# Kernel optimization log

Hardware: AMD Instinct MI355X
Metric: run time of the kernel (lower is better)

Reference implementation:

```python
import jax, jax.numpy as jnp
import numpy as np

NUM_HEADS = 8
KEY_SIZE = 64
VALUE_SIZE = 64
NUM_GROUPS = 3 * NUM_HEADS  # 24
C = NUM_HEADS * (2 * KEY_SIZE + VALUE_SIZE)  # 1536
EPS = 1e-5


def setup_inputs() -> dict:
    key = jax.random.key(0)
    k1, k2, k3 = jax.random.split(key, 3)
    x = jax.random.normal(k1, (8, C, 32, 32), dtype=jnp.float32)
    # GroupNorm affine params (torch default ones/zeros, perturbed for non-trivial grads)
    gn_weight = 1.0 + 0.1 * jax.random.normal(k2, (C,), dtype=jnp.float32)
    gn_bias = 0.1 * jax.random.normal(k3, (C,), dtype=jnp.float32)
    return {"x": x, "gn_weight": gn_weight, "gn_bias": gn_bias}


def _group_norm(x, weight, bias):
    B, Cc, H, W = x.shape
    xg = x.reshape(B, NUM_GROUPS, -1)  # [B, G, (C/G)*H*W]
    mean = jnp.mean(xg, axis=-1, keepdims=True)
    var = jnp.var(xg, axis=-1, keepdims=True)
    xn = ((xg - mean) * jax.lax.rsqrt(var + EPS)).reshape(B, Cc, H, W)
    return xn * weight[:, None, None] + bias[:, None, None]


def reference(x, gn_weight, gn_bias):
    NH, KS, VS = NUM_HEADS, KEY_SIZE, VALUE_SIZE
    B, Cc, H, W = x.shape
    xn = _group_norm(x, gn_weight, gn_bias)
    xr = xn.reshape(B, NH, 2 * KS + VS, H * W)  # [B, NH, 2KS+VS, NK]
    k = xr[:, :, :KS]            # [B, NH, KS, NK]
    q = xr[:, :, KS:2 * KS]      # [B, NH, KS, NK]
    v = xr[:, :, 2 * KS:]        # [B, NH, VS, NK]
    # saliency = q^T @ k / sqrt(KS) -> [B, NH, NKq, NKk]
    sal = jnp.einsum('bhcq,bhck->bhqk', q, k) / jnp.sqrt(jnp.float32(KS))
    mask = jax.nn.softmax(sal, axis=-1)
    # out = v @ mask^T -> [B, NH, VS, NKq]
    out = jnp.einsum('bhvk,bhqk->bhvq', v, mask)
    return out.reshape(B, NH * VS, H, W)
```

## Files before the change

### kernel.cpp

```cpp
#include <hip/hip_runtime.h>
#include <hip/hip_bf16.h>


typedef __attribute__((ext_vector_type(8))) short bf16x8;
typedef __attribute__((ext_vector_type(4))) float f32x4;
typedef __attribute__((ext_vector_type(16))) float f32x16;
typedef unsigned short u16;
typedef unsigned int u32;

#define SM_SCALE 0.18033688f
#define SM_OFF   8.0f

__device__ __forceinline__ u32 pack2(float a, float b) {
    union { float f; u32 u; } ua, ub; ua.f = a; ub.f = b;
    return __builtin_amdgcn_perm(ub.u + 0x8000u, ua.u + 0x8000u, 0x07060302u);
}
union BB { uint4 u; bf16x8 v; };

__device__ __forceinline__ float fexp2(float x) {
#if __has_builtin(__builtin_amdgcn_exp2f)
    return __builtin_amdgcn_exp2f(x);
#else
    float r; asm("v_exp_f32 %0, %1" : "=v"(r) : "v"(x)); return r;
#endif
}

__device__ __forceinline__ f32x16 zero16() {
    f32x16 z;
#pragma unroll
    for (int i = 0; i < 16; ++i) z[i] = 0.f;
    return z;
}

__device__ __forceinline__ void swap32(u32 a, u32 b, int hi, u32& ret0, u32& ret1) {
#if __has_builtin(__builtin_amdgcn_permlane32_swap)
    (void)hi;
    auto sw = __builtin_amdgcn_permlane32_swap(a, b, false, false);
    ret0 = sw[0]; ret1 = sw[1];
#else
    u32 pa = __shfl_xor(a, 32), pb = __shfl_xor(b, 32);
    ret0 = hi ? pb : a;
    ret1 = hi ? b : pa;
#endif
}

__global__ __launch_bounds__(256) void gn_partial(const float* __restrict__ x,
                                                  float* __restrict__ partials) {
    int blk = blockIdx.x;
    const float4* p = (const float4*)(x + (size_t)blk * 8192);
    int t = threadIdx.x;
    float s1a = 0.f, s2a = 0.f, s1b = 0.f, s2b = 0.f;
#pragma unroll
    for (int i = 0; i < 8; i += 2) {
        float4 va = p[t + i * 256];
        float4 vb = p[t + (i + 1) * 256];
        s1a += va.x + va.y + va.z + va.w;
        s2a += va.x*va.x + va.y*va.y + va.z*va.z + va.w*va.w;
        s1b += vb.x + vb.y + vb.z + vb.w;
        s2b += vb.x*vb.x + vb.y*vb.y + vb.z*vb.z + vb.w*vb.w;
    }
    float s1 = s1a + s1b, s2 = s2a + s2b;
    for (int off = 32; off > 0; off >>= 1) {
        s1 += __shfl_down(s1, off);
        s2 += __shfl_down(s2, off);
    }
    __shared__ float a1[4], a2[4];
    int wave = t >> 6, lane = t & 63;
    if (lane == 0) { a1[wave] = s1; a2[wave] = s2; }
    __syncthreads();
    if (t == 0) {
        partials[blk * 2 + 0] = a1[0] + a1[1] + a1[2] + a1[3];
        partials[blk * 2 + 1] = a2[0] + a2[1] + a2[2] + a2[3];
    }
}

__device__ __forceinline__ void group_stats(const float* __restrict__ partials,
                                            int bg, float& mean, float& rstd) {
    float s1 = 0.f, s2 = 0.f;
#pragma unroll
    for (int j = 0; j < 8; ++j) {
        s1 += partials[(bg * 8 + j) * 2 + 0];
        s2 += partials[(bg * 8 + j) * 2 + 1];
    }
    mean = s1 * (1.f / 65536.f);
    float var = s2 * (1.f / 65536.f) - mean * mean;
    rstd = rsqrtf(var + 1e-5f);
}

__global__ __launch_bounds__(512, 2) void attn_fused(
    const float* __restrict__ x, const float* __restrict__ gamma,
    const float* __restrict__ beta, const float* __restrict__ partials,
    float* __restrict__ out)
{
    const int bid = blockIdx.x;
    const int qt = bid >> 6;
    const int pair = bid & 63;
    const int b = pair >> 3, h = pair & 7;
    const float* xb = x + (size_t)b * 1536 * 1024;
    const int tid = threadIdx.x;
    const int w2 = tid >> 6;
    const int lane = tid & 63;
    const int li = lane & 31;
    const int hi = lane >> 5;

    float ms[3], rs[3];
    group_stats(partials, b * 24 + 3 * h + 0, ms[0], rs[0]);
    group_stats(partials, b * 24 + 3 * h + 1, ms[1], rs[1]);
    group_stats(partials, b * 24 + 3 * h + 2, ms[2], rs[2]);

    __shared__ uint4 KT[2][512];
    __shared__ uint4 VT[2][512];

    const int sr  = tid & 63;
    const int kcc = tid >> 6;
    const int kidx = sr * 8 + (kcc ^ (sr & 7));
    const int vc  = tid >> 3;
    const int vs8 = (tid & 7) * 8;
    const int vidx = vc * 8 + ((tid & 7) ^ (vc & 7));

    const float* kbase = xb + (size_t)(h * 192 + kcc * 8) * 1024 + sr;
    const float* vbase = xb + (size_t)(h * 192 + 128 + vc) * 1024 + vs8;

    const int q0 = qt * 256 + w2 * 32;
    bf16x8 bq[4];
    float dqp = 0.f;
#pragma unroll
    for (int cs = 0; cs < 4; ++cs) {
        u32 qq[4];
#pragma unroll
        for (int jp = 0; jp < 4; ++jp) {
            int c0 = cs * 16 + hi * 8 + jp * 2;
            int cgq = h * 192 + 64 + c0;
            int cgk = h * 192 + c0;
            float wq0 = gamma[cgq] * rs[1],     bq0 = beta[cgq] - ms[1] * wq0;
            float wq1 = gamma[cgq + 1] * rs[1], bq1 = beta[cgq + 1] - ms[1] * wq1;
            float wk0 = gamma[cgk] * rs[0],     bk0 = beta[cgk] - ms[0] * wk0;
            float wk1 = gamma[cgk + 1] * rs[0], bk1 = beta[cgk + 1] - ms[0] * wk1;
            float a0 = xb[(size_t)cgq * 1024 + q0 + li];
            float a1 = xb[(size_t)(cgq + 1) * 1024 + q0 + li];
            float qn0 = __builtin_fmaf(a0, wq0, bq0);
            float qn1 = __builtin_fmaf(a1, wq1, bq1);
            dqp = __builtin_fmaf(bk0, qn0, dqp);
            dqp = __builtin_fmaf(bk1, qn1, dqp);
            qq[jp] = pack2(qn0 * wk0, qn1 * wk1);
        }
        BB tb; tb.u = uint4{qq[0], qq[1], qq[2], qq[3]};
        bq[cs] = tb.v;
    }
    const float dq = dqp + __shfl_xor(dqp, 32);
    const float offq = __builtin_fmaf(dq, SM_SCALE, -SM_OFF);

    f32x16 oacc[2];
    oacc[0] = zero16(); oacc[1] = zero16();
    float lsum = 0.f;

    const int x7 = li & 7;

    float rk[8], rv[8];
#define LOAD_TILE(KT_)                                                        \
    {                                                                         \
        const float* kp = kbase + (KT_) * 64;                                 \
        _Pragma("unroll")                                                     \
        for (int u = 0; u < 8; ++u) rk[u] = kp[(size_t)u * 1024];             \
        const float* vp = vbase + (KT_) * 64;                                 \
        float4 v0 = *(const float4*)(vp);                                     \
        float4 v1 = *(const float4*)(vp + 4);                                 \
        rv[0] = v0.x; rv[1] = v0.y; rv[2] = v0.z; rv[3] = v0.w;               \
        rv[4] = v1.x; rv[5] = v1.y; rv[6] = v1.z; rv[7] = v1.w;               \
    }
#define COMMIT_TILE(BUF_)                                                     \
    {                                                                         \
        uint4 ka, va;                                                         \
        ka.x = pack2(rk[0], rk[1]); ka.y = pack2(rk[2], rk[3]);               \
        ka.z = pack2(rk[4], rk[5]); ka.w = pack2(rk[6], rk[7]);               \
        va.x = pack2(rv[0], rv[1]); va.y = pack2(rv[2], rv[3]);               \
        va.z = pack2(rv[4], rv[5]); va.w = pack2(rv[6], rv[7]);               \
        KT[BUF_][kidx] = ka; VT[BUF_][vidx] = va;                             \
    }

    LOAD_TILE(0);
    COMMIT_TILE(0);
    __syncthreads();

#pragma unroll 2
    for (int kt = 0; kt < 16; ++kt) {
        const int cur = kt & 1;
        if (kt < 15) LOAD_TILE(kt + 1);

        BB pbv[4];
#pragma unroll
        for (int kf = 0; kf < 2; ++kf) {
            bf16x8 ak[4];
#pragma unroll
            for (int cs = 0; cs < 4; ++cs)
                ak[cs] = ((const BB*)&KT[cur][(kf * 32 + li) * 8 + ((cs * 2 + hi) ^ x7)])->v;
            f32x16 acc = zero16();
            __builtin_amdgcn_s_setprio(1);
#pragma unroll
            for (int cs = 0; cs < 4; ++cs)
                acc = __builtin_amdgcn_mfma_f32_32x32x16_bf16(ak[cs], bq[cs], acc, 0, 0, 0);
            __builtin_amdgcn_s_setprio(0);
#pragma unroll
            for (int s = 0; s < 2; ++s) {
                float p0 = fexp2(__builtin_fmaf(acc[8 * s + 0], SM_SCALE, offq));
                float p1 = fexp2(__builtin_fmaf(acc[8 * s + 1], SM_SCALE, offq));
                float p2 = fexp2(__builtin_fmaf(acc[8 * s + 2], SM_SCALE, offq));
                float p3 = fexp2(__builtin_fmaf(acc[8 * s + 3], SM_SCALE, offq));
                float p4 = fexp2(__builtin_fmaf(acc[8 * s + 4], SM_SCALE, offq));
                float p5 = fexp2(__builtin_fmaf(acc[8 * s + 5], SM_SCALE, offq));
                float p6 = fexp2(__builtin_fmaf(acc[8 * s + 6], SM_SCALE, offq));
                float p7 = fexp2(__builtin_fmaf(acc[8 * s + 7], SM_SCALE, offq));
                lsum += ((p0 + p1) + (p2 + p3)) + ((p4 + p5) + (p6 + p7));
                u32 Pa = pack2(p0, p1), Pb = pack2(p2, p3);
                u32 Pc = pack2(p4, p5), Pd = pack2(p6, p7);
                u32 w0, w1, w2m, w3;
                swap32(Pa, Pc, hi, w0, w2m);
                swap32(Pb, Pd, hi, w1, w3);
                pbv[kf * 2 + s].u = uint4{w0, w1, w2m, w3};
            }
        }

#pragma unroll
        for (int vf = 0; vf < 2; ++vf) {
            bf16x8 av[4];
#pragma unroll
            for (int ks = 0; ks < 4; ++ks)
                av[ks] = ((const BB*)&VT[cur][(vf * 32 + li) * 8 + ((ks * 2 + hi) ^ x7)])->v;
            __builtin_amdgcn_s_setprio(1);
#pragma unroll
            for (int ks = 0; ks < 4; ++ks)
                oacc[vf] = __builtin_amdgcn_mfma_f32_32x32x16_bf16(av[ks], pbv[ks].v, oacc[vf], 0, 0, 0);
            __builtin_amdgcn_s_setprio(0);
        }

        if (kt < 15) COMMIT_TILE(cur ^ 1);
        __syncthreads();
    }

    lsum += __shfl_xor(lsum, 32);
    float invl = 1.f / lsum;
    float* ob = out + (size_t)pair * 65536 + q0 + li;
#pragma unroll
    for (int vf = 0; vf < 2; ++vf)
#pragma unroll
        for (int r = 0; r < 16; ++r) {
            int v = vf * 32 + (r & 3) + 8 * (r >> 2) + 4 * hi;
            int cgv = h * 192 + 128 + v;
            float wv = gamma[cgv] * rs[2];
            float bvv = beta[cgv] - ms[2] * wv;
            ob[(size_t)v * 1024] = __builtin_fmaf(oacc[vf][r] * invl, wv, bvv);
        }
}

extern "C" void kernel_launch(void* const* d_in, const int* in_sizes, int n_in,
                              void* d_out, int out_size, void* d_ws, size_t ws_size,
                              hipStream_t stream) {
    const float* x     = (const float*)d_in[0];
    const float* gamma = (const float*)d_in[1];
    const float* beta  = (const float*)d_in[2];
    float* out = (float*)d_out;

    float* partials = (float*)d_ws;

    gn_partial<<<1536, 256, 0, stream>>>(x, partials);
    attn_fused<<<256, 512, 0, stream>>>(x, gamma, beta, partials, out);
}
```

Baseline: 116.9 us.

## Fuse GroupNorm statistics into attention kernel, removing separate partial-sum launch

Drops the separate gn_partial kernel and the workspace partials buffer. Each attention block now reads its head's full 192-channel slab itself and computes the three group means and rstds with a block reduction. This removes one kernel launch and the dependency between the two kernels. In exchange the statistics are recomputed redundantly by each of the 4 query-tile blocks per (batch, head), so each block reads an extra 786KB before it starts attention.

```diff
diff --git a/kernel.cpp b/kernel.cpp
--- a/kernel.cpp
+++ b/kernel.cpp
@@ -44,53 +44,9 @@
 #endif
 }
 
-__global__ __launch_bounds__(256) void gn_partial(const float* __restrict__ x,
-                                                  float* __restrict__ partials) {
-    int blk = blockIdx.x;
-    const float4* p = (const float4*)(x + (size_t)blk * 8192);
-    int t = threadIdx.x;
-    float s1a = 0.f, s2a = 0.f, s1b = 0.f, s2b = 0.f;
-#pragma unroll
-    for (int i = 0; i < 8; i += 2) {
-        float4 va = p[t + i * 256];
-        float4 vb = p[t + (i + 1) * 256];
-        s1a += va.x + va.y + va.z + va.w;
-        s2a += va.x*va.x + va.y*va.y + va.z*va.z + va.w*va.w;
-        s1b += vb.x + vb.y + vb.z + vb.w;
-        s2b += vb.x*vb.x + vb.y*vb.y + vb.z*vb.z + vb.w*vb.w;
-    }
-    float s1 = s1a + s1b, s2 = s2a + s2b;
-    for (int off = 32; off > 0; off >>= 1) {
-        s1 += __shfl_down(s1, off);
-        s2 += __shfl_down(s2, off);
-    }
-    __shared__ float a1[4], a2[4];
-    int wave = t >> 6, lane = t & 63;
-    if (lane == 0) { a1[wave] = s1; a2[wave] = s2; }
-    __syncthreads();
-    if (t == 0) {
-        partials[blk * 2 + 0] = a1[0] + a1[1] + a1[2] + a1[3];
-        partials[blk * 2 + 1] = a2[0] + a2[1] + a2[2] + a2[3];
-    }
-}
-
-__device__ __forceinline__ void group_stats(const float* __restrict__ partials,
-                                            int bg, float& mean, float& rstd) {
-    float s1 = 0.f, s2 = 0.f;
-#pragma unroll
-    for (int j = 0; j < 8; ++j) {
-        s1 += partials[(bg * 8 + j) * 2 + 0];
-        s2 += partials[(bg * 8 + j) * 2 + 1];
-    }
-    mean = s1 * (1.f / 65536.f);
-    float var = s2 * (1.f / 65536.f) - mean * mean;
-    rstd = rsqrtf(var + 1e-5f);
-}
-
 __global__ __launch_bounds__(512, 2) void attn_fused(
     const float* __restrict__ x, const float* __restrict__ gamma,
-    const float* __restrict__ beta, const float* __restrict__ partials,
-    float* __restrict__ out)
+    const float* __restrict__ beta, float* __restrict__ out)
 {
     const int bid = blockIdx.x;
     const int qt = bid >> 6;
@@ -103,10 +59,40 @@
     const int li = lane & 31;
     const int hi = lane >> 5;
 
+    const float4* p4 = (const float4*)(xb + (size_t)(h * 192) * 1024);
+    float s1[3] = {0.f, 0.f, 0.f}, s2[3] = {0.f, 0.f, 0.f};
+#pragma unroll
+    for (int g = 0; g < 3; ++g) {
+#pragma unroll 4
+        for (int i2 = 0; i2 < 32; ++i2) {
+            float4 v = p4[(g * 32 + i2) * 512 + tid];
+            s1[g] += (v.x + v.y) + (v.z + v.w);
+            s2[g] += (v.x * v.x + v.y * v.y) + (v.z * v.z + v.w * v.w);
+        }
+    }
+#pragma unroll
+    for (int off = 32; off > 0; off >>= 1)
+#pragma unroll
+        for (int g = 0; g < 3; ++g) {
+            s1[g] += __shfl_down(s1[g], off);
+            s2[g] += __shfl_down(s2[g], off);
+        }
+    __shared__ float red[8][6];
+    if (lane == 0) {
+#pragma unroll
+        for (int g = 0; g < 3; ++g) { red[w2][2 * g] = s1[g]; red[w2][2 * g + 1] = s2[g]; }
+    }
+    __syncthreads();
     float ms[3], rs[3];
-    group_stats(partials, b * 24 + 3 * h + 0, ms[0], rs[0]);
-    group_stats(partials, b * 24 + 3 * h + 1, ms[1], rs[1]);
-    group_stats(partials, b * 24 + 3 * h + 2, ms[2], rs[2]);
+#pragma unroll
+    for (int g = 0; g < 3; ++g) {
+        float a = 0.f, c2 = 0.f;
+#pragma unroll
+        for (int wv = 0; wv < 8; ++wv) { a += red[wv][2 * g]; c2 += red[wv][2 * g + 1]; }
+        float mean = a * (1.f / 65536.f);
+        ms[g] = mean;
+        rs[g] = rsqrtf(c2 * (1.f / 65536.f) - mean * mean + 1e-5f);
+    }
 
     __shared__ uint4 KT[2][512];
     __shared__ uint4 VT[2][512];
@@ -259,9 +245,7 @@
     const float* gamma = (const float*)d_in[1];
     const float* beta  = (const float*)d_in[2];
     float* out = (float*)d_out;
-
-    float* partials = (float*)d_ws;
-
-    gn_partial<<<1536, 256, 0, stream>>>(x, partials);
-    attn_fused<<<256, 512, 0, stream>>>(x, gamma, beta, partials, out);
-}
+    (void)d_ws; (void)ws_size;
+
+    attn_fused<<<256, 512, 0, stream>>>(x, gamma, beta, out);
+}
```

Measured after the change: 128.3 us. 1.1x slower.
